# Kernel optimization log

Hardware: AMD Instinct MI355X
Metric: run time of the kernel (lower is better)

## Reference

```python
import jax, jax.numpy as jnp
import numpy as np

N_NODES = 20000
N_EDGES = 160000
F_IN = 128
H1 = 1024  # 128 * out_channels
H2 = 512   # 64 * out_channels
OUT = 8    # out_channels


def graph_conv(x, src, dst, w_rel, b_rel, w_root):
    # PyG GraphConv(aggr='mean'): out = lin_rel(mean_{j->i} x_j) + lin_root(x_i)
    n = x.shape[0]
    agg = jax.ops.segment_sum(x[src], dst, num_segments=n)          # [N, F_in]
    deg = jax.ops.segment_sum(jnp.ones((src.shape[0],), x.dtype), dst, num_segments=n)
    mean = agg / jnp.maximum(deg, 1.0)[:, None]
    return mean @ w_rel + b_rel + x @ w_root


def setup_inputs() -> dict:
    key = jax.random.key(0)
    ks = jax.random.split(key, 12)
    x = jax.random.normal(ks[0], (N_NODES, F_IN), dtype=jnp.float32)
    edge_index = jax.random.randint(ks[1], (2, N_EDGES), 0, N_NODES, dtype=jnp.int64)

    def lin(k, fi, fo):
        return jax.random.normal(k, (fi, fo), dtype=jnp.float32) / np.sqrt(fi)

    return {
        "x": x,
        "edge_index": edge_index,
        "w1_rel": lin(ks[2], F_IN, H1), "b1": jnp.zeros((H1,), jnp.float32), "w1_root": lin(ks[3], F_IN, H1),
        "w2_rel": lin(ks[4], H1, H2), "b2": jnp.zeros((H2,), jnp.float32), "w2_root": lin(ks[5], H1, H2),
        "wmu_rel": lin(ks[6], H2, OUT), "bmu": jnp.zeros((OUT,), jnp.float32), "wmu_root": lin(ks[7], H2, OUT),
        "wls_rel": lin(ks[8], H2, OUT), "bls": jnp.zeros((OUT,), jnp.float32), "wls_root": lin(ks[9], H2, OUT),
    }


def reference(x, edge_index, w1_rel, b1, w1_root, w2_rel, b2, w2_root,
              wmu_rel, bmu, wmu_root, wls_rel, bls, wls_root):
    src, dst = edge_index[0], edge_index[1]
    h = jax.nn.relu(graph_conv(x, src, dst, w1_rel, b1, w1_root))
    h = jax.nn.relu(graph_conv(h, src, dst, w2_rel, b2, w2_root))
    mu = graph_conv(h, src, dst, wmu_rel, bmu, wmu_root)
    logstd = graph_conv(h, src, dst, wls_rel, bls, wls_root)
    return (mu, logstd)
```

## Files before the change

kernel.cpp:

```cpp
#include <hip/hip_runtime.h>

typedef __attribute__((ext_vector_type(8))) short short8;
typedef __attribute__((ext_vector_type(4))) float f32x4;
typedef unsigned long long u64;

__device__ __forceinline__ unsigned short f2bf(float f) {
  union { float f; unsigned u; } v; v.f = f;
  unsigned u = v.u;
  unsigned r = (u + 0x7FFFu + ((u >> 16) & 1u)) >> 16;
  return (unsigned short)r;
}
__device__ __forceinline__ float bf2f(unsigned short s) {
  union { unsigned u; float f; } v; v.u = ((unsigned)s) << 16;
  return v.f;
}

__device__ __forceinline__ void gl_lds16(const unsigned short* g, unsigned short* l) {
  __builtin_amdgcn_global_load_lds(
      (const __attribute__((address_space(1))) void*)g,
      (__attribute__((address_space(3))) void*)l, 16, 0, 0);
}


__global__ void zero_int_kernel(int* a, int n, int* b, int nb, int* flag) {
  int i = blockIdx.x * blockDim.x + threadIdx.x;
  int stride = gridDim.x * blockDim.x;
  for (int j = i; j < n; j += stride) a[j] = 0;
  for (int j = i; j < nb; j += stride) b[j] = 0;
  if (i == 0) *flag = 1;
}

__global__ void detect_kernel(const long long* p, int nslots, int n_nodes, int* flag) {
  int i = blockIdx.x * blockDim.x + threadIdx.x;
  if (i < nslots) {
    long long v = p[i];
    if (v < 0 || v >= n_nodes) atomicAnd(flag, 0);
  }
}

__device__ __forceinline__ int edge_at(const void* p, int is64, size_t idx) {
  return is64 ? (int)((const long long*)p)[idx] : ((const int*)p)[idx];
}

__global__ void count_kernel(const void* edges, int E, const int* flag, int* deg) {
  int is64 = *flag;
  int i = blockIdx.x * blockDim.x + threadIdx.x;
  int stride = gridDim.x * blockDim.x;
  for (int e = i; e < E; e += stride) {
    int d = edge_at(edges, is64, (size_t)E + e);
    atomicAdd(&deg[d], 1);
  }
}

__global__ void scan_kernel(const int* __restrict__ deg, int* __restrict__ rs,
                            float* __restrict__ invdeg, int n) {
  __shared__ int ssum[1024];
  int tid = threadIdx.x;
  int chunk = (n + 1023) >> 10;
  int start = tid * chunk;
  int end = min(start + chunk, n);
  int s = 0;
  for (int i = start; i < end; ++i) s += deg[i];
  ssum[tid] = s;
  __syncthreads();
  for (int off = 1; off < 1024; off <<= 1) {
    int t = (tid >= off) ? ssum[tid - off] : 0;
    __syncthreads();
    ssum[tid] += t;
    __syncthreads();
  }
  int run = (tid ? ssum[tid - 1] : 0);
  if (tid == 0) rs[0] = 0;
  for (int i = start; i < end; ++i) {
    int d = deg[i];
    run += d;
    rs[i + 1] = run;
    invdeg[i] = 1.0f / fmaxf((float)d, 1.0f);
  }
}

__global__ void fill_kernel(const void* edges, int E, const int* flag,
                            const int* __restrict__ rs, int* cursor, int* col_src) {
  int is64 = *flag;
  int i = blockIdx.x * blockDim.x + threadIdx.x;
  int stride = gridDim.x * blockDim.x;
  for (int e = i; e < E; e += stride) {
    int d = edge_at(edges, is64, (size_t)E + e);
    int s = edge_at(edges, is64, (size_t)e);
    int p = atomicAdd(&cursor[d], 1);
    col_src[rs[d] + p] = s;
  }
}


__global__ void cast_x_kernel(const float* __restrict__ x, unsigned short* __restrict__ A,
                              int total4, int F, int lda, int coloff) {
  int i = blockIdx.x * blockDim.x + threadIdx.x;
  int stride = gridDim.x * blockDim.x;
  for (int idx = i; idx < total4; idx += stride) {
    const float4 v = reinterpret_cast<const float4*>(x)[idx];
    int flat = idx * 4;
    int row = flat / F, f = flat % F;
    ushort4 o;
    o.x = f2bf(v.x); o.y = f2bf(v.y); o.z = f2bf(v.z); o.w = f2bf(v.w);
    *reinterpret_cast<ushort4*>(&A[(size_t)row * lda + coloff + f]) = o;
  }
}

__global__ void agg_f32_kernel(const float* __restrict__ x, int F,
                               const int* __restrict__ rs, const int* __restrict__ cs,
                               const float* __restrict__ invdeg,
                               unsigned short* __restrict__ out, int ldo) {
  int node = blockIdx.x;
  int f = threadIdx.x;
  float acc = 0.f;
  int e1 = rs[node + 1];
  for (int e = rs[node]; e < e1; ++e) {
    int s = cs[e];
    acc += x[(size_t)s * F + f];
  }
  out[(size_t)node * ldo + f] = f2bf(acc * invdeg[node]);
}

__global__ void agg2_kernel(const unsigned short* __restrict__ P2,
                            const int* __restrict__ rs, const int* __restrict__ cs,
                            const float* __restrict__ invdeg,
                            const float* __restrict__ b2,
                            unsigned short* __restrict__ h2) {
  int node = blockIdx.x;
  int f0 = threadIdx.x * 4;
  float acc0 = 0.f, acc1 = 0.f, acc2 = 0.f, acc3 = 0.f;
  int e1 = rs[node + 1];
  for (int e = rs[node]; e < e1; ++e) {
    int s = cs[e];
    u64 w = *reinterpret_cast<const u64*>(P2 + (size_t)s * 1024 + f0);
    acc0 += bf2f((unsigned short)w);
    acc1 += bf2f((unsigned short)(w >> 16));
    acc2 += bf2f((unsigned short)(w >> 32));
    acc3 += bf2f((unsigned short)(w >> 48));
  }
  float inv = invdeg[node];
  u64 wr = *reinterpret_cast<const u64*>(P2 + (size_t)node * 1024 + 512 + f0);
  float v0 = fmaxf(acc0 * inv + bf2f((unsigned short)wr) + b2[f0 + 0], 0.f);
  float v1 = fmaxf(acc1 * inv + bf2f((unsigned short)(wr >> 16)) + b2[f0 + 1], 0.f);
  float v2 = fmaxf(acc2 * inv + bf2f((unsigned short)(wr >> 32)) + b2[f0 + 2], 0.f);
  float v3 = fmaxf(acc3 * inv + bf2f((unsigned short)(wr >> 48)) + b2[f0 + 3], 0.f);
  u64 o = (u64)f2bf(v0) | ((u64)f2bf(v1) << 16) | ((u64)f2bf(v2) << 32) | ((u64)f2bf(v3) << 48);
  *reinterpret_cast<u64*>(h2 + (size_t)node * 512 + f0) = o;
}

__global__ void head_agg_kernel(const float* __restrict__ P3,
                                const int* __restrict__ rs, const int* __restrict__ cs,
                                const float* __restrict__ invdeg,
                                const float* __restrict__ bmu, const float* __restrict__ bls,
                                float* __restrict__ outmu, float* __restrict__ outls, int M) {
  int idx = blockIdx.x * blockDim.x + threadIdx.x;
  int node = idx >> 4;
  int c = idx & 15;
  if (node >= M) return;
  int relc = (c < 8) ? c : (16 + (c - 8));
  float acc = 0.f;
  int e1 = rs[node + 1];
  for (int e = rs[node]; e < e1; ++e) acc += P3[(size_t)cs[e] * 128 + relc];
  float v = acc * invdeg[node] + P3[(size_t)node * 128 + relc + 8]
          + ((c < 8) ? bmu[c] : bls[c - 8]);
  if (c < 8) outmu[(size_t)node * 8 + c] = v;
  else outls[(size_t)node * 8 + (c - 8)] = v;
}


__global__ void wtrans_kernel(const float* __restrict__ w_rel, const float* __restrict__ w_root,
                              int F, int Nout, unsigned short* __restrict__ Bt) {
  int total = Nout * 2 * F;
  int i = blockIdx.x * blockDim.x + threadIdx.x;
  int stride = gridDim.x * blockDim.x;
  for (int idx = i; idx < total; idx += stride) {
    int n = idx / (2 * F);
    int k = idx % (2 * F);
    float v = (k < F) ? w_rel[(size_t)k * Nout + n] : w_root[(size_t)(k - F) * Nout + n];
    Bt[idx] = f2bf(v);
  }
}

__global__ void wtrans2_kernel(const float* __restrict__ w_rel, const float* __restrict__ w_root,
                               int K, int Half, unsigned short* __restrict__ Bt) {
  int total = 2 * Half * K;
  int i = blockIdx.x * blockDim.x + threadIdx.x;
  int stride = gridDim.x * blockDim.x;
  for (int idx = i; idx < total; idx += stride) {
    int n = idx / K;
    int k = idx % K;
    float v = (n < Half) ? w_rel[(size_t)k * Half + n] : w_root[(size_t)k * Half + (n - Half)];
    Bt[idx] = f2bf(v);
  }
}

__global__ void wtrans_heads_kernel(const float* __restrict__ wmu_rel, const float* __restrict__ wmu_root,
                                    const float* __restrict__ wls_rel, const float* __restrict__ wls_root,
                                    int K, unsigned short* __restrict__ Bt) {
  int total = 128 * K;
  int i = blockIdx.x * blockDim.x + threadIdx.x;
  int stride = gridDim.x * blockDim.x;
  for (int idx = i; idx < total; idx += stride) {
    int n = idx / K;
    int k = idx % K;
    float v = 0.f;
    if (n < 8) v = wmu_rel[(size_t)k * 8 + n];
    else if (n < 16) v = wmu_root[(size_t)k * 8 + (n - 8)];
    else if (n < 24) v = wls_rel[(size_t)k * 8 + (n - 16)];
    else if (n < 32) v = wls_root[(size_t)k * 8 + (n - 24)];
    Bt[idx] = f2bf(v);
  }
}

__launch_bounds__(256, 3)
__global__ void gemm_kernel(const unsigned short* __restrict__ A, int lda,
                            const unsigned short* __restrict__ Bt, int ldb,
                            const float* __restrict__ bias,
                            void* __restrict__ outp, int ldo,
                            int M, int N, int K, int relu, int out_f32, int gx) {
  __shared__ unsigned short As[2 * 128 * 32];
  __shared__ unsigned short Bs[2 * 128 * 32];
  int tid = threadIdx.x;
  int lane = tid & 63;
  int w = tid >> 6;
  int wr = w >> 1, wc = w & 1;
  int lr = lane & 15, lk = lane >> 4;

  int nwg = gridDim.x;
  int orig = blockIdx.x;
  int q = nwg >> 3, r = nwg & 7;
  int xcd = orig & 7, lid = orig >> 3;
  int swz = (xcd < r ? xcd * (q + 1) : r * (q + 1) + (xcd - r) * q) + lid;
  int m0 = (swz / gx) * 128, n0 = (swz % gx) * 128;

  f32x4 acc[4][4];
#pragma unroll
  for (int i = 0; i < 4; ++i)
#pragma unroll
    for (int j = 0; j < 4; ++j) acc[i][j] = (f32x4)0.0f;

  int srow = tid >> 2;
  int scol = (tid & 3) * 8;
  const unsigned short* gA = A + (size_t)(m0 + srow) * lda + scol;
  const unsigned short* gB = Bt + (size_t)(n0 + srow) * ldb + scol;
  size_t a64 = (size_t)64 * lda, b64 = (size_t)64 * ldb;
  unsigned short* lA = As + w * 512;
  unsigned short* lB = Bs + w * 512;

  gl_lds16(gA, lA); gl_lds16(gA + a64, lA + 2048);
  gl_lds16(gB, lB); gl_lds16(gB + b64, lB + 2048);
  gA += 32; gB += 32;
  __syncthreads();

  int nt = K >> 5;
  for (int t = 0; t < nt; ++t) {
    int cur = (t & 1) * 4096;
    if (t + 1 < nt) {
      int nxt = cur ^ 4096;
      gl_lds16(gA, lA + nxt); gl_lds16(gA + a64, lA + nxt + 2048);
      gl_lds16(gB, lB + nxt); gl_lds16(gB + b64, lB + nxt + 2048);
      gA += 32; gB += 32;
    }
    const unsigned short* as_ = As + cur;
    const unsigned short* bs_ = Bs + cur;
    short8 af[4], bfr[4];
#pragma unroll
    for (int i = 0; i < 4; ++i) {
      af[i]  = *reinterpret_cast<const short8*>(&as_[(wr * 64 + i * 16 + lr) * 32 + lk * 8]);
      bfr[i] = *reinterpret_cast<const short8*>(&bs_[(wc * 64 + i * 16 + lr) * 32 + lk * 8]);
    }
#pragma unroll
    for (int i = 0; i < 4; ++i)
#pragma unroll
      for (int j = 0; j < 4; ++j)
        acc[i][j] = __builtin_amdgcn_mfma_f32_16x16x32_bf16(af[i], bfr[j], acc[i][j], 0, 0, 0);
    __syncthreads();
  }

#pragma unroll
  for (int i = 0; i < 4; ++i) {
    int row_b = m0 + wr * 64 + i * 16 + lk * 4;
#pragma unroll
    for (int j = 0; j < 4; ++j) {
      int col = n0 + wc * 64 + j * 16 + lr;
      float bv = bias ? bias[col] : 0.f;
#pragma unroll
      for (int r = 0; r < 4; ++r) {
        int row = row_b + r;
        if (row < M) {
          float v = acc[i][j][r] + bv;
          if (relu) v = fmaxf(v, 0.f);
          if (out_f32) ((float*)outp)[(size_t)row * ldo + col] = v;
          else ((unsigned short*)outp)[(size_t)row * ldo + col] = f2bf(v);
        }
      }
    }
  }
}


extern "C" void kernel_launch(void* const* d_in, const int* in_sizes, int n_in,
                              void* d_out, int out_size, void* d_ws, size_t ws_size,
                              hipStream_t stream) {
  const float* x = (const float*)d_in[0];
  const void* edge = d_in[1];
  const float* w1_rel = (const float*)d_in[2];
  const float* b1 = (const float*)d_in[3];
  const float* w1_root = (const float*)d_in[4];
  const float* w2_rel = (const float*)d_in[5];
  const float* b2 = (const float*)d_in[6];
  const float* w2_root = (const float*)d_in[7];
  const float* wmu_rel = (const float*)d_in[8];
  const float* bmu = (const float*)d_in[9];
  const float* wmu_root = (const float*)d_in[10];
  const float* wls_rel = (const float*)d_in[11];
  const float* bls = (const float*)d_in[12];
  const float* wls_root = (const float*)d_in[13];

  const int FIN = 128, H1 = 1024, H2 = 512;
  const int M = in_sizes[0] / FIN;
  const int E = in_sizes[1] / 2;
  const int Mpad = ((M + 127) / 128) * 128;
  const int gy = Mpad / 128;

  char* ws = (char*)d_ws;
  size_t off = 0;
  auto alloc = [&](size_t bytes) -> char* {
    char* p = ws + off;
    off = (off + bytes + 255) & ~(size_t)255;
    return p;
  };
  int* flag = (int*)alloc(4);
  int* deg = (int*)alloc((size_t)M * 4);
  int* cursor = (int*)alloc((size_t)M * 4);
  int* rs = (int*)alloc((size_t)(M + 1) * 4);
  float* invdeg = (float*)alloc((size_t)M * 4);
  int* cs = (int*)alloc((size_t)E * 4);
  unsigned short* A1 = (unsigned short*)alloc((size_t)Mpad * 256 * 2);
  unsigned short* h1 = (unsigned short*)alloc((size_t)Mpad * 1024 * 2);
  unsigned short* P2 = (unsigned short*)alloc((size_t)Mpad * 1024 * 2);
  unsigned short* h2 = (unsigned short*)alloc((size_t)Mpad * 512 * 2);
  float* P3 = (float*)alloc((size_t)Mpad * 128 * 4);
  unsigned short* Bt1 = (unsigned short*)alloc((size_t)H1 * 256 * 2);
  unsigned short* Bt2 = (unsigned short*)alloc((size_t)1024 * 1024 * 2);
  unsigned short* Bt3 = (unsigned short*)alloc((size_t)128 * 512 * 2);

  zero_int_kernel<<<64, 256, 0, stream>>>(deg, M, cursor, M, flag);
  detect_kernel<<<8, 256, 0, stream>>>((const long long*)edge, 2048, M, flag);
  count_kernel<<<256, 256, 0, stream>>>(edge, E, flag, deg);
  scan_kernel<<<1, 1024, 0, stream>>>(deg, rs, invdeg, M);
  fill_kernel<<<256, 256, 0, stream>>>(edge, E, flag, rs, cursor, cs);

  wtrans_kernel<<<256, 256, 0, stream>>>(w1_rel, w1_root, FIN, H1, Bt1);
  wtrans2_kernel<<<512, 256, 0, stream>>>(w2_rel, w2_root, H1, H2, Bt2);
  wtrans_heads_kernel<<<64, 256, 0, stream>>>(wmu_rel, wmu_root, wls_rel, wls_root, H2, Bt3);

  cast_x_kernel<<<640, 256, 0, stream>>>(x, A1, M * FIN / 4, FIN, 256, FIN);
  agg_f32_kernel<<<M, 128, 0, stream>>>(x, FIN, rs, cs, invdeg, A1, 256);
  gemm_kernel<<<(H1 / 128) * gy, 256, 0, stream>>>(
      A1, 256, Bt1, 256, b1, h1, 1024, M, H1, 256, 1, 0, H1 / 128);

  gemm_kernel<<<(1024 / 128) * gy, 256, 0, stream>>>(
      h1, 1024, Bt2, 1024, nullptr, P2, 1024, M, 1024, 1024, 0, 0, 1024 / 128);
  agg2_kernel<<<M, 128, 0, stream>>>(P2, rs, cs, invdeg, b2, h2);

  gemm_kernel<<<1 * gy, 256, 0, stream>>>(
      h2, 512, Bt3, 512, nullptr, P3, 128, M, 128, 512, 0, 1, 1);
  float* outmu = (float*)d_out;
  float* outls = outmu + (size_t)M * 8;
  head_agg_kernel<<<(M * 16 + 255) / 256, 256, 0, stream>>>(
      P3, rs, cs, invdeg, bmu, bls, outmu, outls, M);
}
```

Before: 291.3 us.

## Triple-buffer GEMM with LDS swizzle, fuse weight transposes and small kernels

The GEMM moves from double to triple buffering of LDS tiles, with explicit vmcnt waits and raw barriers so global-to-LDS loads run two steps ahead. An XOR swizzle on the LDS layout reduces bank conflicts, and s_setprio raises priority around the MFMA block. Separately, the three weight-transpose kernels merge into one that uses a shared-memory tiled transpose for coalesced access. The init and detect kernels merge, and the x cast folds into the layer-1 aggregation, which cuts launches. In exchange the GEMM uses more LDS, which may lower occupancy.

Result: faster. 278.0 us (-4.6%).

```diff
diff --git a/kernel.cpp b/kernel.cpp
--- a/kernel.cpp
+++ b/kernel.cpp
@@ -22,18 +22,15 @@
 }
 
 
-__global__ void zero_int_kernel(int* a, int n, int* b, int nb, int* flag) {
+__global__ void init_kernel(int* a, int n, int* b, int nb, int* flag,
+                            const long long* edges, int nslots, int n_nodes) {
   int i = blockIdx.x * blockDim.x + threadIdx.x;
   int stride = gridDim.x * blockDim.x;
   for (int j = i; j < n; j += stride) a[j] = 0;
   for (int j = i; j < nb; j += stride) b[j] = 0;
   if (i == 0) *flag = 1;
-}
-
-__global__ void detect_kernel(const long long* p, int nslots, int n_nodes, int* flag) {
-  int i = blockIdx.x * blockDim.x + threadIdx.x;
-  if (i < nslots) {
-    long long v = p[i];
+  for (int j = i; j < nslots; j += stride) {
+    long long v = edges[j];
     if (v < 0 || v >= n_nodes) atomicAnd(flag, 0);
   }
 }
@@ -93,33 +90,20 @@
 }
 
 
-__global__ void cast_x_kernel(const float* __restrict__ x, unsigned short* __restrict__ A,
-                              int total4, int F, int lda, int coloff) {
-  int i = blockIdx.x * blockDim.x + threadIdx.x;
-  int stride = gridDim.x * blockDim.x;
-  for (int idx = i; idx < total4; idx += stride) {
-    const float4 v = reinterpret_cast<const float4*>(x)[idx];
-    int flat = idx * 4;
-    int row = flat / F, f = flat % F;
-    ushort4 o;
-    o.x = f2bf(v.x); o.y = f2bf(v.y); o.z = f2bf(v.z); o.w = f2bf(v.w);
-    *reinterpret_cast<ushort4*>(&A[(size_t)row * lda + coloff + f]) = o;
-  }
-}
-
-__global__ void agg_f32_kernel(const float* __restrict__ x, int F,
-                               const int* __restrict__ rs, const int* __restrict__ cs,
-                               const float* __restrict__ invdeg,
-                               unsigned short* __restrict__ out, int ldo) {
+__global__ void agg1_kernel(const float* __restrict__ x,
+                            const int* __restrict__ rs, const int* __restrict__ cs,
+                            const float* __restrict__ invdeg,
+                            unsigned short* __restrict__ A1) {
   int node = blockIdx.x;
   int f = threadIdx.x;
+  float xi = x[(size_t)node * 128 + f];
   float acc = 0.f;
   int e1 = rs[node + 1];
   for (int e = rs[node]; e < e1; ++e) {
-    int s = cs[e];
-    acc += x[(size_t)s * F + f];
-  }
-  out[(size_t)node * ldo + f] = f2bf(acc * invdeg[node]);
+    acc += x[(size_t)cs[e] * 128 + f];
+  }
+  A1[(size_t)node * 256 + f] = f2bf(acc * invdeg[node]);
+  A1[(size_t)node * 256 + 128 + f] = f2bf(xi);
 }
 
 __global__ void agg2_kernel(const unsigned short* __restrict__ P2,
@@ -169,47 +153,45 @@
 }
 
 
-__global__ void wtrans_kernel(const float* __restrict__ w_rel, const float* __restrict__ w_root,
-                              int F, int Nout, unsigned short* __restrict__ Bt) {
-  int total = Nout * 2 * F;
-  int i = blockIdx.x * blockDim.x + threadIdx.x;
-  int stride = gridDim.x * blockDim.x;
-  for (int idx = i; idx < total; idx += stride) {
-    int n = idx / (2 * F);
-    int k = idx % (2 * F);
-    float v = (k < F) ? w_rel[(size_t)k * Nout + n] : w_root[(size_t)(k - F) * Nout + n];
-    Bt[idx] = f2bf(v);
-  }
-}
-
-__global__ void wtrans2_kernel(const float* __restrict__ w_rel, const float* __restrict__ w_root,
-                               int K, int Half, unsigned short* __restrict__ Bt) {
-  int total = 2 * Half * K;
-  int i = blockIdx.x * blockDim.x + threadIdx.x;
-  int stride = gridDim.x * blockDim.x;
-  for (int idx = i; idx < total; idx += stride) {
-    int n = idx / K;
-    int k = idx % K;
-    float v = (n < Half) ? w_rel[(size_t)k * Half + n] : w_root[(size_t)k * Half + (n - Half)];
-    Bt[idx] = f2bf(v);
-  }
-}
-
-__global__ void wtrans_heads_kernel(const float* __restrict__ wmu_rel, const float* __restrict__ wmu_root,
-                                    const float* __restrict__ wls_rel, const float* __restrict__ wls_root,
-                                    int K, unsigned short* __restrict__ Bt) {
-  int total = 128 * K;
-  int i = blockIdx.x * blockDim.x + threadIdx.x;
-  int stride = gridDim.x * blockDim.x;
-  for (int idx = i; idx < total; idx += stride) {
-    int n = idx / K;
-    int k = idx % K;
-    float v = 0.f;
+__device__ __forceinline__ void ttile(const float* __restrict__ src, int Nw,
+                                      unsigned short* __restrict__ dst, int ldd,
+                                      int rowoff, int coloff,
+                                      int tileIdx, int tilesN, float (*tile)[33]) {
+  int tk = tileIdx / tilesN, tn = tileIdx % tilesN;
+  int k0 = tk * 32, n0 = tn * 32;
+  int tx = threadIdx.x & 31, ty = threadIdx.x >> 5;
+#pragma unroll
+  for (int s = 0; s < 4; ++s)
+    tile[ty + s * 8][tx] = src[(size_t)(k0 + ty + s * 8) * Nw + n0 + tx];
+  __syncthreads();
+#pragma unroll
+  for (int s = 0; s < 4; ++s)
+    dst[(size_t)(rowoff + n0 + ty + s * 8) * ldd + coloff + k0 + tx] =
+        f2bf(tile[tx][ty + s * 8]);
+}
+
+__global__ void wtrans_all_kernel(const float* __restrict__ w1_rel, const float* __restrict__ w1_root,
+                                  const float* __restrict__ w2_rel, const float* __restrict__ w2_root,
+                                  const float* __restrict__ wmu_rel, const float* __restrict__ wmu_root,
+                                  const float* __restrict__ wls_rel, const float* __restrict__ wls_root,
+                                  unsigned short* __restrict__ Bt1,
+                                  unsigned short* __restrict__ Bt2,
+                                  unsigned short* __restrict__ Bt3) {
+  __shared__ float tile[32][33];
+  int b = blockIdx.x;
+  if (b < 128)       ttile(w1_rel, 1024, Bt1, 256, 0, 0, b, 32, tile);
+  else if (b < 256)  ttile(w1_root, 1024, Bt1, 256, 0, 128, b - 128, 32, tile);
+  else if (b < 768)  ttile(w2_rel, 512, Bt2, 1024, 0, 0, b - 256, 16, tile);
+  else if (b < 1280) ttile(w2_root, 512, Bt2, 1024, 512, 0, b - 768, 16, tile);
+  else {
+    int idx = (b - 1280) * 256 + threadIdx.x;
+    int n = idx >> 9, k = idx & 511;
+    float v;
     if (n < 8) v = wmu_rel[(size_t)k * 8 + n];
     else if (n < 16) v = wmu_root[(size_t)k * 8 + (n - 8)];
     else if (n < 24) v = wls_rel[(size_t)k * 8 + (n - 16)];
-    else if (n < 32) v = wls_root[(size_t)k * 8 + (n - 24)];
-    Bt[idx] = f2bf(v);
+    else v = wls_root[(size_t)k * 8 + (n - 24)];
+    Bt3[(size_t)n * 512 + k] = f2bf(v);
   }
 }
 
@@ -219,16 +201,15 @@
                             const float* __restrict__ bias,
                             void* __restrict__ outp, int ldo,
                             int M, int N, int K, int relu, int out_f32, int gx) {
-  __shared__ unsigned short As[2 * 128 * 32];
-  __shared__ unsigned short Bs[2 * 128 * 32];
+  __shared__ unsigned short As[3 * 4096];
+  __shared__ unsigned short Bs[3 * 4096];
   int tid = threadIdx.x;
   int lane = tid & 63;
   int w = tid >> 6;
   int wr = w >> 1, wc = w & 1;
   int lr = lane & 15, lk = lane >> 4;
 
-  int nwg = gridDim.x;
-  int orig = blockIdx.x;
+  int nwg = gridDim.x, orig = blockIdx.x;
   int q = nwg >> 3, r = nwg & 7;
   int xcd = orig & 7, lid = orig >> 3;
   int swz = (xcd < r ? xcd * (q + 1) : r * (q + 1) + (xcd - r) * q) + lid;
@@ -240,42 +221,59 @@
 #pragma unroll
     for (int j = 0; j < 4; ++j) acc[i][j] = (f32x4)0.0f;
 
-  int srow = tid >> 2;
-  int scol = (tid & 3) * 8;
-  const unsigned short* gA = A + (size_t)(m0 + srow) * lda + scol;
-  const unsigned short* gB = Bt + (size_t)(n0 + srow) * ldb + scol;
+  int r0 = tid >> 2;
+  int slog = (tid & 3) ^ ((r0 >> 1) & 3);
+  const unsigned short* gA = A + (size_t)(m0 + r0) * lda + slog * 8;
+  const unsigned short* gB = Bt + (size_t)(n0 + r0) * ldb + slog * 8;
   size_t a64 = (size_t)64 * lda, b64 = (size_t)64 * ldb;
-  unsigned short* lA = As + w * 512;
-  unsigned short* lB = Bs + w * 512;
-
-  gl_lds16(gA, lA); gl_lds16(gA + a64, lA + 2048);
-  gl_lds16(gB, lB); gl_lds16(gB + b64, lB + 2048);
+  unsigned short* wa = As + w * 512;
+  unsigned short* wb = Bs + w * 512;
+
+  int sw8 = (lk ^ ((lr >> 1) & 3)) * 8;
+
+  int nt = K >> 5;
+  gl_lds16(gA, wa); gl_lds16(gA + a64, wa + 2048);
+  gl_lds16(gB, wb); gl_lds16(gB + b64, wb + 2048);
   gA += 32; gB += 32;
-  __syncthreads();
-
-  int nt = K >> 5;
+  gl_lds16(gA, wa + 4096); gl_lds16(gA + a64, wa + 6144);
+  gl_lds16(gB, wb + 4096); gl_lds16(gB + b64, wb + 6144);
+  gA += 32; gB += 32;
+  asm volatile("s_waitcnt vmcnt(4)" ::: "memory");
+  __builtin_amdgcn_s_barrier();
+
+  int bufR = 0, bufS = 2;
   for (int t = 0; t < nt; ++t) {
-    int cur = (t & 1) * 4096;
-    if (t + 1 < nt) {
-      int nxt = cur ^ 4096;
-      gl_lds16(gA, lA + nxt); gl_lds16(gA + a64, lA + nxt + 2048);
-      gl_lds16(gB, lB + nxt); gl_lds16(gB + b64, lB + nxt + 2048);
+    if (t + 2 < nt) {
+      unsigned short* sa = As + bufS * 4096 + w * 512;
+      unsigned short* sb = Bs + bufS * 4096 + w * 512;
+      gl_lds16(gA, sa); gl_lds16(gA + a64, sa + 2048);
+      gl_lds16(gB, sb); gl_lds16(gB + b64, sb + 2048);
       gA += 32; gB += 32;
     }
-    const unsigned short* as_ = As + cur;
-    const unsigned short* bs_ = Bs + cur;
+    const unsigned short* as_ = As + bufR * 4096;
+    const unsigned short* bs_ = Bs + bufR * 4096;
     short8 af[4], bfr[4];
 #pragma unroll
     for (int i = 0; i < 4; ++i) {
-      af[i]  = *reinterpret_cast<const short8*>(&as_[(wr * 64 + i * 16 + lr) * 32 + lk * 8]);
-      bfr[i] = *reinterpret_cast<const short8*>(&bs_[(wc * 64 + i * 16 + lr) * 32 + lk * 8]);
+      af[i]  = *reinterpret_cast<const short8*>(&as_[(wr * 64 + i * 16 + lr) * 32 + sw8]);
+      bfr[i] = *reinterpret_cast<const short8*>(&bs_[(wc * 64 + i * 16 + lr) * 32 + sw8]);
     }
+    __builtin_amdgcn_s_setprio(1);
 #pragma unroll
     for (int i = 0; i < 4; ++i)
 #pragma unroll
       for (int j = 0; j < 4; ++j)
         acc[i][j] = __builtin_amdgcn_mfma_f32_16x16x32_bf16(af[i], bfr[j], acc[i][j], 0, 0, 0);
-    __syncthreads();
+    __builtin_amdgcn_s_setprio(0);
+    if (t + 1 < nt) {
+      if (t + 2 < nt)
+        asm volatile("s_waitcnt vmcnt(4) lgkmcnt(0)" ::: "memory");
+      else
+        asm volatile("s_waitcnt vmcnt(0) lgkmcnt(0)" ::: "memory");
+      __builtin_amdgcn_s_barrier();
+    }
+    bufR = (bufR == 2) ? 0 : bufR + 1;
+    bufS = (bufS == 2) ? 0 : bufS + 1;
   }
 
 #pragma unroll
@@ -286,10 +284,10 @@
       int col = n0 + wc * 64 + j * 16 + lr;
       float bv = bias ? bias[col] : 0.f;
 #pragma unroll
-      for (int r = 0; r < 4; ++r) {
-        int row = row_b + r;
+      for (int rr = 0; rr < 4; ++rr) {
+        int row = row_b + rr;
         if (row < M) {
-          float v = acc[i][j][r] + bv;
+          float v = acc[i][j][rr] + bv;
           if (relu) v = fmaxf(v, 0.f);
           if (out_f32) ((float*)outp)[(size_t)row * ldo + col] = v;
           else ((unsigned short*)outp)[(size_t)row * ldo + col] = f2bf(v);
@@ -346,18 +344,16 @@
   unsigned short* Bt2 = (unsigned short*)alloc((size_t)1024 * 1024 * 2);
   unsigned short* Bt3 = (unsigned short*)alloc((size_t)128 * 512 * 2);
 
-  zero_int_kernel<<<64, 256, 0, stream>>>(deg, M, cursor, M, flag);
-  detect_kernel<<<8, 256, 0, stream>>>((const long long*)edge, 2048, M, flag);
+  init_kernel<<<64, 256, 0, stream>>>(deg, M, cursor, M, flag, (const long long*)edge, 2048, M);
   count_kernel<<<256, 256, 0, stream>>>(edge, E, flag, deg);
   scan_kernel<<<1, 1024, 0, stream>>>(deg, rs, invdeg, M);
   fill_kernel<<<256, 256, 0, stream>>>(edge, E, flag, rs, cursor, cs);
 
-  wtrans_kernel<<<256, 256, 0, stream>>>(w1_rel, w1_root, FIN, H1, Bt1);
-  wtrans2_kernel<<<512, 256, 0, stream>>>(w2_rel, w2_root, H1, H2, Bt2);
-  wtrans_heads_kernel<<<64, 256, 0, stream>>>(wmu_rel, wmu_root, wls_rel, wls_root, H2, Bt3);
-
-  cast_x_kernel<<<640, 256, 0, stream>>>(x, A1, M * FIN / 4, FIN, 256, FIN);
-  agg_f32_kernel<<<M, 128, 0, stream>>>(x, FIN, rs, cs, invdeg, A1, 256);
+  wtrans_all_kernel<<<1344, 256, 0, stream>>>(w1_rel, w1_root, w2_rel, w2_root,
+                                              wmu_rel, wmu_root, wls_rel, wls_root,
+                                              Bt1, Bt2, Bt3);
+
+  agg1_kernel<<<M, 128, 0, stream>>>(x, rs, cs, invdeg, A1);
   gemm_kernel<<<(H1 / 128) * gy, 256, 0, stream>>>(
       A1, 256, Bt1, 256, b1, h1, 1024, M, H1, 256, 1, 0, H1 / 128);
 
```
